# Performance work log

Hardware: AMD Instinct MI355X
Metric: run time of the kernel (lower is better)

Reference implementation:

```python
import jax, jax.numpy as jnp
import numpy as np

B, S, H = 32768, 16, 16  # batch, seq_len, G_hiddensize (code requires H == S and H == latent_dim == 16)
LATENT = 16
DISC_DIMS = [(1, 32), (32, 16), (16, 8), (8, 16), (16, 32)]


def setup_inputs() -> dict:
    key = jax.random.key(0)
    ks = iter(jax.random.split(key, 64))
    def p(shape, scale=0.1):
        return (jax.random.normal(next(ks), shape, dtype=jnp.float32) * scale)
    inp = dict(
        values=jax.random.normal(next(ks), (B, S), dtype=jnp.float32),
        masks=jax.random.randint(next(ks), (B, S), 0, 2).astype(jnp.int32),
        g_fwd_Wih=p((4 * H, 1)), g_fwd_Whh=p((4 * H, H)), g_fwd_b=p((4 * H,)),
        g_bwd_Wih=p((4 * H, 1)), g_bwd_Whh=p((4 * H, H)), g_bwd_b=p((4 * H,)),
        imp_W=p((1, H)), imp_b=p((1,)),
        fc_W=p((LATENT, H)), fc_b=p((LATENT,)),
        dec_Wih=p((4 * H, LATENT)), dec_Whh=p((4 * H, H)), dec_b=p((4 * H,)),
        dec_out_W=p((1, H)), dec_out_b=p((1,)),
        disc_out_W=p((1, 32)), disc_out_b=p((1,)),
    )
    for k, (i, h) in enumerate(DISC_DIMS):
        inp[f"d_W_{k}"] = p((4 * h, i))
        inp[f"d_b_{k}"] = p((4 * h,))
    return inp


def lstm_cell(x, h, c, Wih, Whh, b):
    gates = x @ Wih.T + h @ Whh.T + b
    i, f, g, o = jnp.split(gates, 4, axis=-1)
    c = jax.nn.sigmoid(f) * c + jax.nn.sigmoid(i) * jnp.tanh(g)
    h = jax.nn.sigmoid(o) * jnp.tanh(c)
    return h, c


def _forward(values, masks, g_fwd_Wih, g_fwd_Whh, g_fwd_b, g_bwd_Wih, g_bwd_Whh, g_bwd_b,
             imp_W, imp_b, fc_W, fc_b, dec_Wih, dec_Whh, dec_b, dec_out_W, dec_out_b,
             disc_out_W, disc_out_b,
             d_W_0, d_b_0, d_W_1, d_b_1, d_W_2, d_b_2, d_W_3, d_b_3, d_W_4, d_b_4):
    dt = values.dtype
    Bsz = values.shape[0]
    x = values[:, :, None]                     # (B, S, 1)
    m = masks.astype(dt)[:, :, None]           # (B, S, 1)
    # NOTE: torch.flip along axis 2 (size 1) is a no-op, so the bwd cell sees the
    # same (un-reversed) sequence as the fwd cell -- faithfully reproduced here.
    zH = jnp.zeros((Bsz, H), dt)
    h_f, c_f = lstm_cell(jnp.full((Bsz, 1), 128.0, dt), zH, zH, g_fwd_Wih, g_fwd_Whh, g_fwd_b)
    h_b, c_b = lstm_cell(jnp.full((Bsz, 1), -128.0, dt), zH, zH, g_bwd_Wih, g_bwd_Whh, g_bwd_b)

    def gen_step(carry, xm):
        h_f, c_f, h_b, c_b = carry
        x_t, m_t = xm                          # (B,1) each
        cc_f = (1 - m_t) * x_t + m_t * (h_f @ imp_W.T + imp_b)
        cc_b = (1 - m_t) * x_t + m_t * (h_b @ imp_W.T + imp_b)
        h_f, c_f = lstm_cell(cc_f, h_f, c_f, g_fwd_Wih, g_fwd_Whh, g_fwd_b)
        h_b, c_b = lstm_cell(cc_b, h_b, c_b, g_bwd_Wih, g_bwd_Whh, g_bwd_b)
        return (h_f, c_f, h_b, c_b), None

    (h_f, c_f, h_b, c_b), _ = jax.lax.scan(
        gen_step, (h_f, c_f, h_b, c_b),
        (jnp.transpose(x, (1, 0, 2)), jnp.transpose(m, (1, 0, 2))))
    h = h_f + h_b                               # (B, H), H == S
    imputations = h.reshape(Bsz, S, 1)
    imputed = imputations * (1 - m) + x * m      # (B, S, 1)

    # Discriminator: torch calls each LSTMCell WITHOUT state every timestep, so
    # hidden/cell start at zero each call -> purely feedforward per (batch, t).
    # W_hh @ 0 == 0, so only W_ih and the combined bias matter. Vectorize over B*S.
    inp = imputed.reshape(Bsz * S, 1)
    for W, b in ((d_W_0, d_b_0), (d_W_1, d_b_1), (d_W_2, d_b_2), (d_W_3, d_b_3), (d_W_4, d_b_4)):
        gates = inp @ W.T + b
        i, f, g, o = jnp.split(gates, 4, axis=-1)
        cc = jax.nn.sigmoid(i) * jnp.tanh(g)
        inp = jax.nn.sigmoid(o) * jnp.tanh(cc)
    disc_output = (inp @ disc_out_W.T + disc_out_b).reshape(Bsz, S, 1)

    latent = h @ fc_W.T + fc_b                  # (B, 16)

    # Decoder: ignores latent values (only uses batch size); start token = 128s.
    hd = cd = jnp.zeros((Bsz, H), dt)
    hd, cd = lstm_cell(jnp.full((Bsz, LATENT), 128.0, dt), hd, cd, dec_Wih, dec_Whh, dec_b)

    def dec_step(carry, _):
        hd, cd = carry
        hd, cd = lstm_cell(cd, hd, cd, dec_Wih, dec_Whh, dec_b)
        return (hd, cd), hd @ dec_out_W.T + dec_out_b

    _, outs = jax.lax.scan(dec_step, (hd, cd), None, length=S)  # (S, B, 1)
    reconstructed = jnp.transpose(outs, (1, 0, 2))
    return imputed, disc_output, latent, reconstructed


def reference(values, masks, g_fwd_Wih, g_fwd_Whh, g_fwd_b, g_bwd_Wih, g_bwd_Whh, g_bwd_b,
              imp_W, imp_b, fc_W, fc_b, dec_Wih, dec_Whh, dec_b, dec_out_W, dec_out_b,
              disc_out_W, disc_out_b,
              d_W_0, d_b_0, d_W_1, d_b_1, d_W_2, d_b_2, d_W_3, d_b_3, d_W_4, d_b_4):
    return _forward(values, masks, g_fwd_Wih, g_fwd_Whh, g_fwd_b, g_bwd_Wih, g_bwd_Whh, g_bwd_b,
                    imp_W, imp_b, fc_W, fc_b, dec_Wih, dec_Whh, dec_b, dec_out_W, dec_out_b,
                    disc_out_W, disc_out_b,
                    d_W_0, d_b_0, d_W_1, d_b_1, d_W_2, d_b_2, d_W_3, d_b_3, d_W_4, d_b_4)
```

## Files before the change

kernel.cpp:

```cpp
#include <hip/hip_runtime.h>

#define BB 32768
#define BS (BB*16)

typedef float v2f __attribute__((ext_vector_type(2)));

__device__ __forceinline__ v2f pk_fma(v2f a, v2f b, v2f c){
    v2f d;
    asm("v_pk_fma_f32 %0, %1, %2, %3" : "=v"(d) : "v"(a), "v"(b), "v"(c));
    return d;
}
__device__ __forceinline__ v2f pk_fma_lo(v2f a, v2f b, v2f c){
    v2f d;
    asm("v_pk_fma_f32 %0, %1, %2, %3 op_sel:[0,0,0] op_sel_hi:[0,1,1]"
        : "=v"(d) : "v"(a), "v"(b), "v"(c));
    return d;
}
__device__ __forceinline__ v2f pk_fma_hi(v2f a, v2f b, v2f c){
    v2f d;
    asm("v_pk_fma_f32 %0, %1, %2, %3 op_sel:[1,0,0] op_sel_hi:[1,1,1]"
        : "=v"(d) : "v"(a), "v"(b), "v"(c));
    return d;
}

#define RECO 64
#define TAB  128
#define NTAB 2049
#define HFO  8448
#define HBO  (HFO+BS)

#define PW0 0
#define PB0 96
#define PW1 192
#define PB1 1920
#define PW2 1968
#define PB2 2448
#define PW3 2472
#define PB3 3048
#define PW4 3096
#define PB4 5016
#define POW 5112
#define POB 5144
#define PN  5148

__device__ __forceinline__ float sigm(float x){
    return __builtin_amdgcn_rcpf(1.f + __expf(-x));
}
__device__ __forceinline__ float tanh_f(float x){
    return 1.f - 2.f * __builtin_amdgcn_rcpf(1.f + __expf(2.f * x));
}
__device__ __forceinline__ float dunit(float gi, float gg, float go){
    return sigm(go) * tanh_f(sigm(gi) * tanh_f(gg));
}

struct P29 { const float* p[29]; };

__global__ __launch_bounds__(256)
void k_lstm(P29 a, const int* __restrict__ masks, float* __restrict__ ws)
{
    __shared__ __align__(16) float smem[1040];
    int tid = threadIdx.x;
    int lane = tid & 63;
    int gbase = lane & 48;
    int u = tid & 15;
    int setw = tid >> 4;
    int gid = blockIdx.x * 16 + setw;
    int dir = gid >> 15;
    int b = gid & 32767;
    const float* __restrict__ Whh = a.p[3 + 3*dir];
    v2f wif[16], wgo[16];
    #pragma unroll
    for (int q = 0; q < 4; q++) {
        float4 vi = ((const float4*)(Whh + (u)*16))[q];
        float4 vf = ((const float4*)(Whh + (16+u)*16))[q];
        float4 vg = ((const float4*)(Whh + (32+u)*16))[q];
        float4 vo = ((const float4*)(Whh + (48+u)*16))[q];
        wif[4*q+0] = (v2f){vi.x, vf.x}; wgo[4*q+0] = (v2f){vg.x, vo.x};
        wif[4*q+1] = (v2f){vi.y, vf.y}; wgo[4*q+1] = (v2f){vg.y, vo.y};
        wif[4*q+2] = (v2f){vi.z, vf.z}; wgo[4*q+2] = (v2f){vg.z, vo.z};
        wif[4*q+3] = (v2f){vi.w, vf.w}; wgo[4*q+3] = (v2f){vg.w, vo.w};
    }
    const float* __restrict__ Wih = a.p[2 + 3*dir];
    const float* __restrict__ bia = a.p[4 + 3*dir];
    v2f xif = (v2f){Wih[u], Wih[16+u]}, xgo = (v2f){Wih[32+u], Wih[48+u]};
    v2f bif = (v2f){bia[u], bia[16+u]}, bgo = (v2f){bia[32+u], bia[48+u]};
    v2f impw2[8];
    #pragma unroll
    for (int q = 0; q < 4; q++) {
        float4 v = ((const float4*)a.p[8])[q];
        impw2[2*q+0] = (v2f){v.x, v.y};
        impw2[2*q+1] = (v2f){v.z, v.w};
    }
    float impb = a.p[9][0];
    float x_own = a.p[0][(size_t)b*16 + u];
    int   m_own = masks[(size_t)b*16 + u];
    unsigned mm = (unsigned)(__ballot(m_own != 0) >> gbase) & 0xffffu;
    int xo = 768 + setw*17;
    smem[xo + u] = x_own;
    float sgn = dir ? -128.f : 128.f;
    float giI = sgn*xif.x + bif.x, ggI = sgn*xgo.x + bgo.x, goI = sgn*xgo.y + bgo.y;
    float c = sigm(giI) * tanh_f(ggI);
    float h = sigm(goI) * tanh_f(c);
    int wa = setw*48 + u;
    int ra = setw*12;
    const float4* lhv = (const float4*)smem;
    #pragma unroll
    for (int t = 0; t < 16; t++) {
        smem[wa] = h;
        float4 h0 = lhv[ra + 0];
        float4 h1 = lhv[ra + 1];
        float4 h2 = lhv[ra + 2];
        float4 h3 = lhv[ra + 3];
        v2f p0 = (v2f){h0.x, h0.y}, p1 = (v2f){h0.z, h0.w};
        v2f p2 = (v2f){h1.x, h1.y}, p3 = (v2f){h1.z, h1.w};
        v2f p4 = (v2f){h2.x, h2.y}, p5 = (v2f){h2.z, h2.w};
        v2f p6 = (v2f){h3.x, h3.y}, p7 = (v2f){h3.z, h3.w};
        v2f ia = (v2f){impb, 0.f};
        ia = pk_fma(p0, impw2[0], ia); ia = pk_fma(p1, impw2[1], ia);
        ia = pk_fma(p2, impw2[2], ia); ia = pk_fma(p3, impw2[3], ia);
        ia = pk_fma(p4, impw2[4], ia); ia = pk_fma(p5, impw2[5], ia);
        ia = pk_fma(p6, impw2[6], ia); ia = pk_fma(p7, impw2[7], ia);
        float imp = ia.x + ia.y;
        float xt = smem[xo + t];
        float cc = ((mm >> t) & 1u) ? imp : xt;
        v2f ccv = (v2f){cc, cc};
        v2f gif = pk_fma(ccv, xif, bif);
        v2f ggo = pk_fma(ccv, xgo, bgo);
        gif = pk_fma_lo(p0, wif[0],  gif); ggo = pk_fma_lo(p0, wgo[0],  ggo);
        gif = pk_fma_hi(p0, wif[1],  gif); ggo = pk_fma_hi(p0, wgo[1],  ggo);
        gif = pk_fma_lo(p1, wif[2],  gif); ggo = pk_fma_lo(p1, wgo[2],  ggo);
        gif = pk_fma_hi(p1, wif[3],  gif); ggo = pk_fma_hi(p1, wgo[3],  ggo);
        gif = pk_fma_lo(p2, wif[4],  gif); ggo = pk_fma_lo(p2, wgo[4],  ggo);
        gif = pk_fma_hi(p2, wif[5],  gif); ggo = pk_fma_hi(p2, wgo[5],  ggo);
        gif = pk_fma_lo(p3, wif[6],  gif); ggo = pk_fma_lo(p3, wgo[6],  ggo);
        gif = pk_fma_hi(p3, wif[7],  gif); ggo = pk_fma_hi(p3, wgo[7],  ggo);
        gif = pk_fma_lo(p4, wif[8],  gif); ggo = pk_fma_lo(p4, wgo[8],  ggo);
        gif = pk_fma_hi(p4, wif[9],  gif); ggo = pk_fma_hi(p4, wgo[9],  ggo);
        gif = pk_fma_lo(p5, wif[10], gif); ggo = pk_fma_lo(p5, wgo[10], ggo);
        gif = pk_fma_hi(p5, wif[11], gif); ggo = pk_fma_hi(p5, wgo[11], ggo);
        gif = pk_fma_lo(p6, wif[12], gif); ggo = pk_fma_lo(p6, wgo[12], ggo);
        gif = pk_fma_hi(p6, wif[13], gif); ggo = pk_fma_hi(p6, wgo[13], ggo);
        gif = pk_fma_lo(p7, wif[14], gif); ggo = pk_fma_lo(p7, wgo[14], ggo);
        gif = pk_fma_hi(p7, wif[15], gif); ggo = pk_fma_hi(p7, wgo[15], ggo);
        float cn = sigm(gif.y)*c + sigm(gif.x)*tanh_f(ggo.x);
        c = cn;
        h = sigm(ggo.y)*tanh_f(cn);
    }
    ws[HFO + (size_t)dir*BS + (size_t)b*16 + u] = h;
}

__global__ __launch_bounds__(256)
void k_tabdec(P29 a, float* __restrict__ ws)
{
    __shared__ __align__(16) float wl[PN];
    int tid = threadIdx.x;
    if (blockIdx.x < 129) {
#define STAGE(WS, BSi, h, K, padK, wdst, bdst) \
    { const float* Wp = a.p[WS]; const float* Bp = a.p[BSi]; \
      for (int i = tid; i < 3*(h)*(K); i += 256){ \
        int r = i/(K), k = i - r*(K); int g = r/(h), u0 = r - g*(h); \
        int sr = (g==0? u0 : (g==1? 2*(h)+u0 : 3*(h)+u0)); \
        wl[(wdst) + r*(padK) + k] = Wp[sr*(K) + k]; } \
      for (int i = tid; i < 3*(h); i += 256){ \
        int g = i/(h), u0 = i - g*(h); \
        int sr = (g==0? u0 : (g==1? 2*(h)+u0 : 3*(h)+u0)); \
        wl[(bdst) + i] = Bp[sr]; } }
        STAGE(19, 20, 32,  1,  1, PW0, PB0)
        STAGE(21, 22, 16, 32, 36, PW1, PB1)
        STAGE(23, 24,  8, 16, 20, PW2, PB2)
        STAGE(25, 26, 16,  8, 12, PW3, PB3)
        STAGE(27, 28, 32, 16, 20, PW4, PB4)
#undef STAGE
        { const float* s = a.p[17]; for (int i = tid; i < 32; i += 256) wl[POW+i] = s[i]; }
        if (tid == 0) wl[POB] = a.p[18][0];
        __syncthreads();
        int u = tid & 15;
        int gbase = (tid & 63) & 48;
        int gid = blockIdx.x * 16 + (tid >> 4);
        const float4* w4 = (const float4*)wl;
        float xin = -8.f + (float)gid * (1.f/128.f);
        float lo = dunit(xin*wl[PW0+u]    + wl[PB0+u],
                         xin*wl[PW0+32+u] + wl[PB0+32+u],
                         xin*wl[PW0+64+u] + wl[PB0+64+u]);
        float hi = dunit(xin*wl[PW0+16+u] + wl[PB0+16+u],
                         xin*wl[PW0+48+u] + wl[PB0+48+u],
                         xin*wl[PW0+80+u] + wl[PB0+80+u]);
        float A0[32];
        #pragma unroll
        for (int k = 0; k < 16; k++) { A0[k] = __shfl(lo, gbase+k); A0[16+k] = __shfl(hi, gbase+k); }
        float gi = wl[PB1+u], gg = wl[PB1+16+u], go = wl[PB1+32+u];
        int bi_ = (PW1 + u*36)>>2, bg_ = (PW1 + (16+u)*36)>>2, bo_ = (PW1 + (32+u)*36)>>2;
        #pragma unroll
        for (int q = 0; q < 8; q++) {
            float4 wi = w4[bi_+q], wg = w4[bg_+q], wo = w4[bo_+q];
            float b0=A0[4*q], b1=A0[4*q+1], b2=A0[4*q+2], b3=A0[4*q+3];
            gi += b0*wi.x + b1*wi.y + b2*wi.z + b3*wi.w;
            gg += b0*wg.x + b1*wg.y + b2*wg.z + b3*wg.w;
            go += b0*wo.x + b1*wo.y + b2*wo.z + b3*wo.w;
        }
        float a1 = dunit(gi, gg, go);
        float A1[16];
        #pragma unroll
        for (int k = 0; k < 16; k++) A1[k] = __shfl(a1, gbase+k);
        int v = u & 7;
        gi = wl[PB2+v]; gg = wl[PB2+8+v]; go = wl[PB2+16+v];
        bi_ = (PW2 + v*20)>>2; bg_ = (PW2 + (8+v)*20)>>2; bo_ = (PW2 + (16+v)*20)>>2;
        #pragma unroll
        for (int q = 0; q < 4; q++) {
            float4 wi = w4[bi_+q], wg = w4[bg_+q], wo = w4[bo_+q];
            float b0=A1[4*q], b1=A1[4*q+1], b2=A1[4*q+2], b3=A1[4*q+3];
            gi += b0*wi.x + b1*wi.y + b2*wi.z + b3*wi.w;
            gg += b0*wg.x + b1*wg.y + b2*wg.z + b3*wg.w;
            go += b0*wo.x + b1*wo.y + b2*wo.z + b3*wo.w;
        }
        float a2 = dunit(gi, gg, go);
        float A2[8];
        #pragma unroll
        for (int k = 0; k < 8; k++) A2[k] = __shfl(a2, gbase+k);
        gi = wl[PB3+u]; gg = wl[PB3+16+u]; go = wl[PB3+32+u];
        bi_ = (PW3 + u*12)>>2; bg_ = (PW3 + (16+u)*12)>>2; bo_ = (PW3 + (32+u)*12)>>2;
        #pragma unroll
        for (int q = 0; q < 2; q++) {
            float4 wi = w4[bi_+q], wg = w4[bg_+q], wo = w4[bo_+q];
            float b0=A2[4*q], b1=A2[4*q+1], b2=A2[4*q+2], b3=A2[4*q+3];
            gi += b0*wi.x + b1*wi.y + b2*wi.z + b3*wi.w;
            gg += b0*wg.x + b1*wg.y + b2*wg.z + b3*wg.w;
            go += b0*wo.x + b1*wo.y + b2*wo.z + b3*wo.w;
        }
        float a3 = dunit(gi, gg, go);
        float A3[16];
        #pragma unroll
        for (int k = 0; k < 16; k++) A3[k] = __shfl(a3, gbase+k);
        float part;
        {
            float g0i = wl[PB4+u], g0g = wl[PB4+32+u], g0o = wl[PB4+64+u];
            float g1i = wl[PB4+16+u], g1g = wl[PB4+48+u], g1o = wl[PB4+80+u];
            int c0i = (PW4 + u*20)>>2,      c0g = (PW4 + (32+u)*20)>>2, c0o = (PW4 + (64+u)*20)>>2;
            int c1i = (PW4 + (16+u)*20)>>2, c1g = (PW4 + (48+u)*20)>>2, c1o = (PW4 + (80+u)*20)>>2;
            #pragma unroll
            for (int q = 0; q < 4; q++) {
                float b0=A3[4*q], b1=A3[4*q+1], b2=A3[4*q+2], b3=A3[4*q+3];
                float4 wi = w4[c0i+q], wg = w4[c0g+q], wo = w4[c0o+q];
                g0i += b0*wi.x + b1*wi.y + b2*wi.z + b3*wi.w;
                g0g += b0*wg.x + b1*wg.y + b2*wg.z + b3*wg.w;
                g0o += b0*wo.x + b1*wo.y + b2*wo.z + b3*wo.w;
                wi = w4[c1i+q]; wg = w4[c1g+q]; wo = w4[c1o+q];
                g1i += b0*wi.x + b1*wi.y + b2*wi.z + b3*wi.w;
                g1g += b0*wg.x + b1*wg.y + b2*wg.z + b3*wg.w;
                g1o += b0*wo.x + b1*wo.y + b2*wo.z + b3*wo.w;
            }
            part = dunit(g0i, g0g, g0o)*wl[POW+u] + dunit(g1i, g1g, g1o)*wl[POW+16+u];
        }
        part += __shfl_xor(part, 1);
        part += __shfl_xor(part, 2);
        part += __shfl_xor(part, 4);
        part += __shfl_xor(part, 8);
        if (u == 0 && gid < NTAB) ws[TAB + gid] = part + wl[POB];
        return;
    }
    {
        float* dh = wl;
        float* dc = wl + 16;
        const float* Wih = a.p[12];
        const float* Whh = a.p[13];
        const float* bb  = a.p[14];
        const float* oW  = a.p[15];
        const float* ob  = a.p[16];
        float wii[16], wff[16], wgg[16], woo[16];
        float vii[16], vff[16], vgg[16], voo[16];
        float bi_r=0, bf_r=0, bg_r=0, bo_r=0;
        if (tid < 16) {
            int uu = tid;
            #pragma unroll
            for (int k = 0; k < 16; k++) {
                wii[k]=Wih[uu*16+k];      vii[k]=Whh[uu*16+k];
                wff[k]=Wih[(16+uu)*16+k]; vff[k]=Whh[(16+uu)*16+k];
                wgg[k]=Wih[(32+uu)*16+k]; vgg[k]=Whh[(32+uu)*16+k];
                woo[k]=Wih[(48+uu)*16+k]; voo[k]=Whh[(48+uu)*16+k];
            }
            bi_r=bb[uu]; bf_r=bb[16+uu]; bg_r=bb[32+uu]; bo_r=bb[48+uu];
            float gi = bi_r, gg = bg_r, go = bo_r;
            #pragma unroll
            for (int k = 0; k < 16; k++) {
                gi += 128.f * wii[k];
                gg += 128.f * wgg[k];
                go += 128.f * woo[k];
            }
            float c0 = sigm(gi) * tanh_f(gg);
            dc[tid] = c0; dh[tid] = sigm(go) * tanh_f(c0);
        }
        __syncthreads();
        for (int t = 0; t < 16; t++) {
            float rx[16], rh[16], cold = 0.f;
            if (tid < 16) {
                #pragma unroll
                for (int k = 0; k < 16; k++) { rx[k] = dc[k]; rh[k] = dh[k]; }
                cold = dc[tid];
            }
            __syncthreads();
            if (tid < 16) {
                float gi = bi_r, gf = bf_r, gg = bg_r, go = bo_r;
                #pragma unroll
                for (int k = 0; k < 16; k++) {
                    gi += rx[k]*wii[k] + rh[k]*vii[k];
                    gf += rx[k]*wff[k] + rh[k]*vff[k];
                    gg += rx[k]*wgg[k] + rh[k]*vgg[k];
                    go += rx[k]*woo[k] + rh[k]*voo[k];
                }
                float cn = sigm(gf)*cold + sigm(gi)*tanh_f(gg);
                dc[tid] = cn; dh[tid] = sigm(go)*tanh_f(cn);
            }
            __syncthreads();
            if (tid == 0) {
                float o = ob[0];
                #pragma unroll
                for (int k = 0; k < 16; k++) o += dh[k] * oW[k];
                ws[RECO + t] = o;
            }
            __syncthreads();
        }
    }
}

__global__ __launch_bounds__(256) void k_post(P29 a, const int* __restrict__ masks,
                                              const float* __restrict__ ws,
                                              float* __restrict__ out)
{
    __shared__ float tab[NTAB];
    __shared__ __align__(16) float fw[256];
    __shared__ __align__(16) float rec[16];
    __shared__ float fb[16];
    int tid = threadIdx.x;
    for (int i = tid; i < NTAB; i += 256) tab[i] = ws[TAB + i];
    fw[tid] = a.p[10][tid];
    if (tid < 16) { fb[tid] = a.p[11][tid]; rec[tid] = ws[RECO + tid]; }
    __syncthreads();
    int T = blockIdx.x * 256 + tid;
    int b = T >> 2;
    int q = T & 3;
    int tq = q * 4;
    const float4* hf4 = (const float4*)(ws + HFO + (size_t)b*16);
    const float4* hb4 = (const float4*)(ws + HBO + (size_t)b*16);
    float4 s0, s1, s2, s3;
    {
        float4 f0=hf4[0], f1=hf4[1], f2=hf4[2], f3=hf4[3];
        float4 g0=hb4[0], g1=hb4[1], g2=hb4[2], g3=hb4[3];
        s0 = make_float4(f0.x+g0.x, f0.y+g0.y, f0.z+g0.z, f0.w+g0.w);
        s1 = make_float4(f1.x+g1.x, f1.y+g1.y, f1.z+g1.z, f1.w+g1.w);
        s2 = make_float4(f2.x+g2.x, f2.y+g2.y, f2.z+g2.z, f2.w+g2.w);
        s3 = make_float4(f3.x+g3.x, f3.y+g3.y, f3.z+g3.z, f3.w+g3.w);
    }
    float4 hq = (q==0) ? s0 : (q==1) ? s1 : (q==2) ? s2 : s3;
    float4 xv = *(const float4*)(a.p[0] + (size_t)b*16 + tq);
    int4   mv = *(const int4*)(masks + (size_t)b*16 + tq);
    float impv[4];
    impv[0] = mv.x ? xv.x : hq.x;
    impv[1] = mv.y ? xv.y : hq.y;
    impv[2] = mv.z ? xv.z : hq.z;
    impv[3] = mv.w ? xv.w : hq.w;
    float latv[4];
    #pragma unroll
    for (int j = 0; j < 4; j++) {
        int t = tq + j;
        const float4* wr = (const float4*)(fw + t*16);
        float4 w0=wr[0], w1=wr[1], w2=wr[2], w3=wr[3];
        float l = fb[t];
        l += s0.x*w0.x + s0.y*w0.y + s0.z*w0.z + s0.w*w0.w;
        l += s1.x*w1.x + s1.y*w1.y + s1.z*w1.z + s1.w*w1.w;
        l += s2.x*w2.x + s2.y*w2.y + s2.z*w2.z + s2.w*w2.w;
        l += s3.x*w3.x + s3.y*w3.y + s3.z*w3.z + s3.w*w3.w;
        latv[j] = l;
    }
    float dv[4];
    #pragma unroll
    for (int j = 0; j < 4; j++) {
        float xx = fminf(fmaxf(impv[j], -8.f), 8.f);
        float f = (xx + 8.f) * 128.f;
        float fi = floorf(f);
        int i = (int)fi; i = i > NTAB-2 ? NTAB-2 : i;
        float w = f - fi;
        dv[j] = fmaf(w, tab[i+1] - tab[i], tab[i]);
    }
    float4 rv = ((const float4*)rec)[q];
    size_t eo = (size_t)b*16 + tq;
    *(float4*)(out + eo)        = make_float4(impv[0], impv[1], impv[2], impv[3]);
    *(float4*)(out + BS + eo)   = make_float4(dv[0], dv[1], dv[2], dv[3]);
    *(float4*)(out + 2*BS + eo) = make_float4(latv[0], latv[1], latv[2], latv[3]);
    *(float4*)(out + 3*BS + eo) = rv;
}

extern "C" void kernel_launch(void* const* d_in, const int* in_sizes, int n_in,
                              void* d_out, int out_size, void* d_ws, size_t ws_size,
                              hipStream_t stream)
{
    float* ws = (float*)d_ws;
    P29 a;
    for (int i = 0; i < 29; i++) a.p[i] = (const float*)d_in[i];
    const int* masks = (const int*)d_in[1];
    k_tabdec<<<130, 256, 0, stream>>>(a, ws);
    k_lstm<<<4096, 256, 0, stream>>>(a, masks, ws);
    k_post<<<(BB*4)/256, 256, 0, stream>>>(a, masks, ws, (float*)d_out);
}
```

Measured before the change: 181.6 us.

## Move generator LSTM recurrence onto bf16 MFMA with 16 sequences per wavefront

The bidirectional generator LSTM now runs on 16x16x32 bf16 MFMA instructions. Each wavefront handles 16 batch rows, with the hidden state packed as bf16 in shared memory and the input scalar folded into the K dimension. This replaces the per-thread packed-FP32 FMA dot products and cuts the launch from 4096 to 1024 blocks. In exchange, weights and hidden states are rounded to bf16, which lowers precision, and each step still needs a serial MFMA for the imputation value before the gate MFMAs.

```diff
diff --git a/kernel.cpp b/kernel.cpp
--- a/kernel.cpp
+++ b/kernel.cpp
@@ -3,25 +3,8 @@
 #define BB 32768
 #define BS (BB*16)
 
-typedef float v2f __attribute__((ext_vector_type(2)));
-
-__device__ __forceinline__ v2f pk_fma(v2f a, v2f b, v2f c){
-    v2f d;
-    asm("v_pk_fma_f32 %0, %1, %2, %3" : "=v"(d) : "v"(a), "v"(b), "v"(c));
-    return d;
-}
-__device__ __forceinline__ v2f pk_fma_lo(v2f a, v2f b, v2f c){
-    v2f d;
-    asm("v_pk_fma_f32 %0, %1, %2, %3 op_sel:[0,0,0] op_sel_hi:[0,1,1]"
-        : "=v"(d) : "v"(a), "v"(b), "v"(c));
-    return d;
-}
-__device__ __forceinline__ v2f pk_fma_hi(v2f a, v2f b, v2f c){
-    v2f d;
-    asm("v_pk_fma_f32 %0, %1, %2, %3 op_sel:[1,0,0] op_sel_hi:[1,1,1]"
-        : "=v"(d) : "v"(a), "v"(b), "v"(c));
-    return d;
-}
+typedef __attribute__((ext_vector_type(8))) short bf8v;
+typedef __attribute__((ext_vector_type(4))) float f4v;
 
 #define RECO 64
 #define TAB  128
@@ -52,101 +35,135 @@
 __device__ __forceinline__ float dunit(float gi, float gg, float go){
     return sigm(go) * tanh_f(sigm(gi) * tanh_f(gg));
 }
+__device__ __forceinline__ unsigned short f2bf(float f){
+    union { float f; unsigned int i; } v; v.f = f;
+    unsigned int x = v.i;
+    unsigned int r = x + 0x7fffu + ((x >> 16) & 1u);
+    return (unsigned short)(r >> 16);
+}
 
 struct P29 { const float* p[29]; };
+
+__device__ __forceinline__ bf8v makeB(const float* Whh, const float* Wih,
+                                      int row, int quad)
+{
+    bf8v B = {0,0,0,0,0,0,0,0};
+    if (quad < 2) {
+        const float4* p = (const float4*)(Whh + row*16 + quad*8);
+        float4 a0 = p[0], a1 = p[1];
+        B[0]=(short)f2bf(a0.x); B[1]=(short)f2bf(a0.y);
+        B[2]=(short)f2bf(a0.z); B[3]=(short)f2bf(a0.w);
+        B[4]=(short)f2bf(a1.x); B[5]=(short)f2bf(a1.y);
+        B[6]=(short)f2bf(a1.z); B[7]=(short)f2bf(a1.w);
+    } else if (quad == 2) {
+        B[0] = (short)f2bf(Wih[row]);
+    }
+    return B;
+}
 
 __global__ __launch_bounds__(256)
 void k_lstm(P29 a, const int* __restrict__ masks, float* __restrict__ ws)
 {
-    __shared__ __align__(16) float smem[1040];
-    int tid = threadIdx.x;
+    __shared__ __align__(16) float smem[2624];
+    int tid  = threadIdx.x;
     int lane = tid & 63;
-    int gbase = lane & 48;
-    int u = tid & 15;
-    int setw = tid >> 4;
-    int gid = blockIdx.x * 16 + setw;
-    int dir = gid >> 15;
-    int b = gid & 32767;
+    int wv   = tid >> 6;
+    int n    = lane & 15;
+    int quad = lane >> 4;
+    int dir  = (int)(blockIdx.x >= 512);
+    int gid0 = blockIdx.x * 64 + wv * 16;
+    int b0   = gid0 & 32767;
+    float* wbase = smem + wv * 656;
+    float* xs    = wbase;
+    int*   msI   = (int*)(wbase + 256);
+    unsigned short* hbp = (unsigned short*)(wbase + 512);
+    float* ccf   = wbase + 640;
+    const int4* hbI = (const int4*)hbp;
+
+    {
+        size_t gbase = (size_t)b0 * 16;
+        int e = lane * 4;
+        float4 xv = *(const float4*)(a.p[0] + gbase + e);
+        int4   mv = *(const int4*)(masks + gbase + e);
+        int sm = lane >> 2;
+        int st = (lane & 3) * 4;
+        xs[(st+0)*16 + sm] = xv.x;  msI[(st+0)*16 + sm] = mv.x;
+        xs[(st+1)*16 + sm] = xv.y;  msI[(st+1)*16 + sm] = mv.y;
+        xs[(st+2)*16 + sm] = xv.z;  msI[(st+2)*16 + sm] = mv.z;
+        xs[(st+3)*16 + sm] = xv.w;  msI[(st+3)*16 + sm] = mv.w;
+    }
+    const float* __restrict__ Wih = a.p[2 + 3*dir];
     const float* __restrict__ Whh = a.p[3 + 3*dir];
-    v2f wif[16], wgo[16];
+    const float* __restrict__ bia = a.p[4 + 3*dir];
+    bf8v Bi = makeB(Whh, Wih, n,      quad);
+    bf8v Bf = makeB(Whh, Wih, 16+n,   quad);
+    bf8v Bg = makeB(Whh, Wih, 32+n,   quad);
+    bf8v Bo = makeB(Whh, Wih, 48+n,   quad);
+    bf8v Bp = {0,0,0,0,0,0,0,0};
+    if (quad < 2) {
+        const float4* p = (const float4*)(a.p[8] + quad*8);
+        float4 a0 = p[0], a1 = p[1];
+        Bp[0]=(short)f2bf(a0.x); Bp[1]=(short)f2bf(a0.y);
+        Bp[2]=(short)f2bf(a0.z); Bp[3]=(short)f2bf(a0.w);
+        Bp[4]=(short)f2bf(a1.x); Bp[5]=(short)f2bf(a1.y);
+        Bp[6]=(short)f2bf(a1.z); Bp[7]=(short)f2bf(a1.w);
+    }
+    float impb = a.p[9][0];
+    float bi_ = bia[n], bf_ = bia[16+n], bg_ = bia[32+n], bo_ = bia[48+n];
+    float sgn = dir ? -128.f : 128.f;
+    float c0, h0;
+    {
+        float gi0 = sgn*Wih[n]    + bi_;
+        float gg0 = sgn*Wih[32+n] + bg_;
+        float go0 = sgn*Wih[48+n] + bo_;
+        c0 = sigm(gi0) * tanh_f(gg0);
+        h0 = sigm(go0) * tanh_f(c0);
+    }
+    float c[4] = {c0, c0, c0, c0};
+    float h[4];
+    {
+        unsigned short hb0 = f2bf(h0);
+        #pragma unroll
+        for (int r = 0; r < 4; r++) hbp[(quad*4+r)*16 + n] = hb0;
+    }
+    const f4v cz = {0.f, 0.f, 0.f, 0.f};
+    const bf8v Az = {0,0,0,0,0,0,0,0};
+    for (int t = 0; t < 16; t++) {
+        union { int4 i4; bf8v b; } au;
+        au.i4 = hbI[(n << 1) | (quad & 1)];
+        bf8v A = (quad < 2) ? au.b : Az;
+        f4v dimp = __builtin_amdgcn_mfma_f32_16x16x32_bf16(A, Bp, cz, 0, 0, 0);
+        float4 xt4 = *(const float4*)(xs + t*16 + quad*4);
+        int4   mt4 = *(const int4*)(msI + t*16 + quad*4);
+        float cc0 = mt4.x ? (dimp[0] + impb) : xt4.x;
+        float cc1 = mt4.y ? (dimp[1] + impb) : xt4.y;
+        float cc2 = mt4.z ? (dimp[2] + impb) : xt4.z;
+        float cc3 = mt4.w ? (dimp[3] + impb) : xt4.w;
+        if (n == 0) {
+            ccf[quad*4+0] = cc0; ccf[quad*4+1] = cc1;
+            ccf[quad*4+2] = cc2; ccf[quad*4+3] = cc3;
+        }
+        if (quad == 2) A[0] = (short)f2bf(ccf[n]);
+        f4v di = __builtin_amdgcn_mfma_f32_16x16x32_bf16(A, Bi, cz, 0, 0, 0);
+        f4v df = __builtin_amdgcn_mfma_f32_16x16x32_bf16(A, Bf, cz, 0, 0, 0);
+        f4v dg = __builtin_amdgcn_mfma_f32_16x16x32_bf16(A, Bg, cz, 0, 0, 0);
+        f4v dO = __builtin_amdgcn_mfma_f32_16x16x32_bf16(A, Bo, cz, 0, 0, 0);
+        #pragma unroll
+        for (int r = 0; r < 4; r++) {
+            float gi = di[r] + bi_;
+            float gf = df[r] + bf_;
+            float gg = dg[r] + bg_;
+            float go = dO[r] + bo_;
+            float cn = sigm(gf)*c[r] + sigm(gi)*tanh_f(gg);
+            c[r] = cn;
+            float hh = sigm(go)*tanh_f(cn);
+            h[r] = hh;
+            hbp[(quad*4+r)*16 + n] = f2bf(hh);
+        }
+    }
+    float* outp = ws + HFO + (size_t)dir*BS + (size_t)b0*16;
     #pragma unroll
-    for (int q = 0; q < 4; q++) {
-        float4 vi = ((const float4*)(Whh + (u)*16))[q];
-        float4 vf = ((const float4*)(Whh + (16+u)*16))[q];
-        float4 vg = ((const float4*)(Whh + (32+u)*16))[q];
-        float4 vo = ((const float4*)(Whh + (48+u)*16))[q];
-        wif[4*q+0] = (v2f){vi.x, vf.x}; wgo[4*q+0] = (v2f){vg.x, vo.x};
-        wif[4*q+1] = (v2f){vi.y, vf.y}; wgo[4*q+1] = (v2f){vg.y, vo.y};
-        wif[4*q+2] = (v2f){vi.z, vf.z}; wgo[4*q+2] = (v2f){vg.z, vo.z};
-        wif[4*q+3] = (v2f){vi.w, vf.w}; wgo[4*q+3] = (v2f){vg.w, vo.w};
-    }
-    const float* __restrict__ Wih = a.p[2 + 3*dir];
-    const float* __restrict__ bia = a.p[4 + 3*dir];
-    v2f xif = (v2f){Wih[u], Wih[16+u]}, xgo = (v2f){Wih[32+u], Wih[48+u]};
-    v2f bif = (v2f){bia[u], bia[16+u]}, bgo = (v2f){bia[32+u], bia[48+u]};
-    v2f impw2[8];
-    #pragma unroll
-    for (int q = 0; q < 4; q++) {
-        float4 v = ((const float4*)a.p[8])[q];
-        impw2[2*q+0] = (v2f){v.x, v.y};
-        impw2[2*q+1] = (v2f){v.z, v.w};
-    }
-    float impb = a.p[9][0];
-    float x_own = a.p[0][(size_t)b*16 + u];
-    int   m_own = masks[(size_t)b*16 + u];
-    unsigned mm = (unsigned)(__ballot(m_own != 0) >> gbase) & 0xffffu;
-    int xo = 768 + setw*17;
-    smem[xo + u] = x_own;
-    float sgn = dir ? -128.f : 128.f;
-    float giI = sgn*xif.x + bif.x, ggI = sgn*xgo.x + bgo.x, goI = sgn*xgo.y + bgo.y;
-    float c = sigm(giI) * tanh_f(ggI);
-    float h = sigm(goI) * tanh_f(c);
-    int wa = setw*48 + u;
-    int ra = setw*12;
-    const float4* lhv = (const float4*)smem;
-    #pragma unroll
-    for (int t = 0; t < 16; t++) {
-        smem[wa] = h;
-        float4 h0 = lhv[ra + 0];
-        float4 h1 = lhv[ra + 1];
-        float4 h2 = lhv[ra + 2];
-        float4 h3 = lhv[ra + 3];
-        v2f p0 = (v2f){h0.x, h0.y}, p1 = (v2f){h0.z, h0.w};
-        v2f p2 = (v2f){h1.x, h1.y}, p3 = (v2f){h1.z, h1.w};
-        v2f p4 = (v2f){h2.x, h2.y}, p5 = (v2f){h2.z, h2.w};
-        v2f p6 = (v2f){h3.x, h3.y}, p7 = (v2f){h3.z, h3.w};
-        v2f ia = (v2f){impb, 0.f};
-        ia = pk_fma(p0, impw2[0], ia); ia = pk_fma(p1, impw2[1], ia);
-        ia = pk_fma(p2, impw2[2], ia); ia = pk_fma(p3, impw2[3], ia);
-        ia = pk_fma(p4, impw2[4], ia); ia = pk_fma(p5, impw2[5], ia);
-        ia = pk_fma(p6, impw2[6], ia); ia = pk_fma(p7, impw2[7], ia);
-        float imp = ia.x + ia.y;
-        float xt = smem[xo + t];
-        float cc = ((mm >> t) & 1u) ? imp : xt;
-        v2f ccv = (v2f){cc, cc};
-        v2f gif = pk_fma(ccv, xif, bif);
-        v2f ggo = pk_fma(ccv, xgo, bgo);
-        gif = pk_fma_lo(p0, wif[0],  gif); ggo = pk_fma_lo(p0, wgo[0],  ggo);
-        gif = pk_fma_hi(p0, wif[1],  gif); ggo = pk_fma_hi(p0, wgo[1],  ggo);
-        gif = pk_fma_lo(p1, wif[2],  gif); ggo = pk_fma_lo(p1, wgo[2],  ggo);
-        gif = pk_fma_hi(p1, wif[3],  gif); ggo = pk_fma_hi(p1, wgo[3],  ggo);
-        gif = pk_fma_lo(p2, wif[4],  gif); ggo = pk_fma_lo(p2, wgo[4],  ggo);
-        gif = pk_fma_hi(p2, wif[5],  gif); ggo = pk_fma_hi(p2, wgo[5],  ggo);
-        gif = pk_fma_lo(p3, wif[6],  gif); ggo = pk_fma_lo(p3, wgo[6],  ggo);
-        gif = pk_fma_hi(p3, wif[7],  gif); ggo = pk_fma_hi(p3, wgo[7],  ggo);
-        gif = pk_fma_lo(p4, wif[8],  gif); ggo = pk_fma_lo(p4, wgo[8],  ggo);
-        gif = pk_fma_hi(p4, wif[9],  gif); ggo = pk_fma_hi(p4, wgo[9],  ggo);
-        gif = pk_fma_lo(p5, wif[10], gif); ggo = pk_fma_lo(p5, wgo[10], ggo);
-        gif = pk_fma_hi(p5, wif[11], gif); ggo = pk_fma_hi(p5, wgo[11], ggo);
-        gif = pk_fma_lo(p6, wif[12], gif); ggo = pk_fma_lo(p6, wgo[12], ggo);
-        gif = pk_fma_hi(p6, wif[13], gif); ggo = pk_fma_hi(p6, wgo[13], ggo);
-        gif = pk_fma_lo(p7, wif[14], gif); ggo = pk_fma_lo(p7, wgo[14], ggo);
-        gif = pk_fma_hi(p7, wif[15], gif); ggo = pk_fma_hi(p7, wgo[15], ggo);
-        float cn = sigm(gif.y)*c + sigm(gif.x)*tanh_f(ggo.x);
-        c = cn;
-        h = sigm(ggo.y)*tanh_f(cn);
-    }
-    ws[HFO + (size_t)dir*BS + (size_t)b*16 + u] = h;
+    for (int r = 0; r < 4; r++) outp[(quad*4+r)*16 + n] = h[r];
 }
 
 __global__ __launch_bounds__(256)
@@ -156,7 +173,7 @@
     int tid = threadIdx.x;
     if (blockIdx.x < 129) {
 #define STAGE(WS, BSi, h, K, padK, wdst, bdst) \
-    { const float* Wp = a.p[WS]; const float* Bp = a.p[BSi]; \
+    { const float* Wp = a.p[WS]; const float* Bp2 = a.p[BSi]; \
       for (int i = tid; i < 3*(h)*(K); i += 256){ \
         int r = i/(K), k = i - r*(K); int g = r/(h), u0 = r - g*(h); \
         int sr = (g==0? u0 : (g==1? 2*(h)+u0 : 3*(h)+u0)); \
@@ -164,7 +181,7 @@
       for (int i = tid; i < 3*(h); i += 256){ \
         int g = i/(h), u0 = i - g*(h); \
         int sr = (g==0? u0 : (g==1? 2*(h)+u0 : 3*(h)+u0)); \
-        wl[(bdst) + i] = Bp[sr]; } }
+        wl[(bdst) + i] = Bp2[sr]; } }
         STAGE(19, 20, 32,  1,  1, PW0, PB0)
         STAGE(21, 22, 16, 32, 36, PW1, PB1)
         STAGE(23, 24,  8, 16, 20, PW2, PB2)
@@ -286,8 +303,8 @@
                 gg += 128.f * wgg[k];
                 go += 128.f * woo[k];
             }
-            float c0 = sigm(gi) * tanh_f(gg);
-            dc[tid] = c0; dh[tid] = sigm(go) * tanh_f(c0);
+            float cd0 = sigm(gi) * tanh_f(gg);
+            dc[tid] = cd0; dh[tid] = sigm(go) * tanh_f(cd0);
         }
         __syncthreads();
         for (int t = 0; t < 16; t++) {
@@ -398,6 +415,6 @@
     for (int i = 0; i < 29; i++) a.p[i] = (const float*)d_in[i];
     const int* masks = (const int*)d_in[1];
     k_tabdec<<<130, 256, 0, stream>>>(a, ws);
-    k_lstm<<<4096, 256, 0, stream>>>(a, masks, ws);
+    k_lstm<<<1024, 256, 0, stream>>>(a, masks, ws);
     k_post<<<(BB*4)/256, 256, 0, stream>>>(a, masks, ws, (float*)d_out);
 }
```

After: 165.9 us. -8.7%, faster.
